# Optimization experiments

Hardware: AMD Instinct MI355X
Metric: run time of the kernel (lower is better)

Reference implementation:

```python
import jax, jax.numpy as jnp
import numpy as np

TAU = 0.2
EPS = 1e-12  # matches torch F.normalize eps


def _l2_normalize(x):
    # F.normalize(x, p=2, dim=1): x / max(||x||, eps)
    norm = jnp.sqrt(jnp.sum(x * x, axis=1, keepdims=True))
    return x / jnp.maximum(norm, EPS)


def setup_inputs() -> dict:
    key = jax.random.key(0)
    k1, k2 = jax.random.split(key)
    N, D = 16384, 256
    z1 = jax.random.normal(k1, (N, D), dtype=jnp.float32)
    z2 = jax.random.normal(k2, (N, D), dtype=jnp.float32)
    return {"z1": z1, "z2": z2}


def reference(z1, z2):
    # semi_loss: f(x) = exp(x / tau) over full cosine-similarity matrix
    h1 = _l2_normalize(z1)
    h2 = _l2_normalize(z2)
    sim = jnp.einsum('nd,md->nm', h1, h2)          # [N, N] cosine similarities
    between = jnp.exp(sim / TAU)                   # f(pair_sim)
    diag = jnp.diagonal(between)                   # positive pairs
    row_sum = jnp.sum(between, axis=1)
    loss = jnp.sum(-jnp.log(diag / (row_sum - diag)))
    return loss
```

## Files before the change

### kernel.cpp

```cpp
#include <hip/hip_runtime.h>
#include <hip/hip_bf16.h>

#define NROWS 16384
#define DDIM  256
#define LOG2E 1.4426950408889634f
#define SCALE 7.213475204444817f

typedef __attribute__((ext_vector_type(4))) float f32x4;
typedef __attribute__((ext_vector_type(2))) float f32x2;
typedef __attribute__((ext_vector_type(4))) int   i32x4;
typedef __attribute__((ext_vector_type(8))) int   i32x8;

#define UNIT_SCALE 0x7F7F7F7F

__global__ __launch_bounds__(256) void prep_kernel(
    const float* __restrict__ z1, const float* __restrict__ z2,
    unsigned char* __restrict__ h1q, unsigned char* __restrict__ h2t,
    float* __restrict__ diag5, float* __restrict__ rowsum) {
  int tid = threadIdx.x;
  int w = tid >> 6, lane = tid & 63;
  int r = blockIdx.x * 4 + w;

  const float4 a = ((const float4*)z1)[r * 64 + lane];
  const float4 b = ((const float4*)z2)[r * 64 + lane];

  float ss1 = a.x * a.x + a.y * a.y + a.z * a.z + a.w * a.w;
  float ss2 = b.x * b.x + b.y * b.y + b.z * b.z + b.w * b.w;
  float dp  = a.x * b.x + a.y * b.y + a.z * b.z + a.w * b.w;
  #pragma unroll
  for (int m = 1; m <= 32; m <<= 1) {
    ss1 += __shfl_xor(ss1, m);
    ss2 += __shfl_xor(ss2, m);
    dp  += __shfl_xor(dp, m);
  }
  float inv1 = 1.0f / fmaxf(sqrtf(ss1), 1e-12f);
  float inv2 = 1.0f / fmaxf(sqrtf(ss2), 1e-12f);
  float s1 = inv1 * SCALE;

  int p1 = __builtin_amdgcn_cvt_pk_fp8_f32(a.x * s1, a.y * s1, 0, false);
  p1     = __builtin_amdgcn_cvt_pk_fp8_f32(a.z * s1, a.w * s1, p1, true);
  int p2 = __builtin_amdgcn_cvt_pk_fp8_f32(b.x * inv2, b.y * inv2, 0, false);
  p2     = __builtin_amdgcn_cvt_pk_fp8_f32(b.z * inv2, b.w * inv2, p2, true);
  ((int*)h1q)[r * 64 + lane] = p1;

  {
    int c = lane >> 2, sub = lane & 3;
    int off = (r >> 4) * 4096 + (c >> 3) * 2048 + (c & 1) * 1024 +
              ((c >> 1) & 3) * 256 + (r & 15) * 16 + sub * 4;
    *(int*)(h2t + off) = p2;
  }

  if (lane == 0) diag5[r] = dp * inv1 * inv2 * 5.0f;
  if (tid < 4) rowsum[blockIdx.x * 4 + tid] = 0.0f;
}

#define CSPL 16

#define LOADSET(B, P0, P1) do { \
  B[0] = *reinterpret_cast<const i32x4*>(P0); \
  B[1] = *reinterpret_cast<const i32x4*>(P0 + 1024); \
  B[2] = *reinterpret_cast<const i32x4*>(P0 + 2048); \
  B[3] = *reinterpret_cast<const i32x4*>(P0 + 3072); \
  B[4] = *reinterpret_cast<const i32x4*>(P1); \
  B[5] = *reinterpret_cast<const i32x4*>(P1 + 1024); \
  B[6] = *reinterpret_cast<const i32x4*>(P1 + 2048); \
  B[7] = *reinterpret_cast<const i32x4*>(P1 + 3072); \
  P0 += 8192; P1 += 8192; } while (0)

#define MFMA_S(Aop, Bop, Cop) \
  __builtin_amdgcn_mfma_scale_f32_16x16x128_f8f6f4( \
      Aop, Bop, Cop, 0, 0, 0, UNIT_SCALE, 0, UNIT_SCALE)

#define COMPUTE(B) do { \
  union { i32x8 v; i32x4 h[2]; } u00, u01, u10, u11; \
  u00.h[0] = B[0]; u00.h[1] = B[1]; u01.h[0] = B[2]; u01.h[1] = B[3]; \
  u10.h[0] = B[4]; u10.h[1] = B[5]; u11.h[0] = B[6]; u11.h[1] = B[7]; \
  f32x4 a0[4], a1[4]; \
  _Pragma("unroll") for (int m = 0; m < 4; ++m) a0[m] = MFMA_S(afr[m][0], u00.v, ZV); \
  _Pragma("unroll") for (int m = 0; m < 4; ++m) a1[m] = MFMA_S(afr[m][0], u10.v, ZV); \
  _Pragma("unroll") for (int m = 0; m < 4; ++m) a0[m] = MFMA_S(afr[m][1], u01.v, a0[m]); \
  _Pragma("unroll") for (int m = 0; m < 4; ++m) a1[m] = MFMA_S(afr[m][1], u11.v, a1[m]); \
  _Pragma("unroll") for (int m = 0; m < 4; ++m) { \
    rs2[m][0] += (f32x2){__builtin_amdgcn_exp2f(a0[m][0]), __builtin_amdgcn_exp2f(a0[m][1])}; \
    rs2[m][1] += (f32x2){__builtin_amdgcn_exp2f(a0[m][2]), __builtin_amdgcn_exp2f(a0[m][3])}; \
    rs2[m][0] += (f32x2){__builtin_amdgcn_exp2f(a1[m][0]), __builtin_amdgcn_exp2f(a1[m][1])}; \
    rs2[m][1] += (f32x2){__builtin_amdgcn_exp2f(a1[m][2]), __builtin_amdgcn_exp2f(a1[m][3])}; \
  } } while (0)

__global__ __launch_bounds__(256) void simexp_kernel(
    const unsigned char* __restrict__ h1q, const unsigned char* __restrict__ h2t,
    float* __restrict__ rowsum) {
  int tid = threadIdx.x, w = tid >> 6, lane = tid & 63;
  int bx = blockIdx.x;
  int rb = bx >> 4;
  int cs = bx & 15;
  int row0 = rb * 256 + w * 64;

  const char* h1b = (const char*)h1q;

  i32x8 afr[4][2];
  #pragma unroll
  for (int m = 0; m < 4; ++m)
    #pragma unroll
    for (int ks = 0; ks < 2; ++ks) {
      int row = row0 + m * 16 + (lane & 15);
      int off = row * 256 + ks * 128 + (lane >> 4) * 32;
      afr[m][ks] = *reinterpret_cast<const i32x8*>(h1b + off);
    }
  #pragma unroll
  for (int m = 0; m < 4; ++m)
    #pragma unroll
    for (int ks = 0; ks < 2; ++ks)
      asm volatile("" : "+v"(afr[m][ks]));

  const char* Bp0 = (const char*)h2t + (size_t)cs * 262144 + lane * 16;
  const char* Bp1 = Bp0 + 4096;

  const f32x4 ZV = {0.f, 0.f, 0.f, 0.f};
  f32x2 rs2[4][2];
  #pragma unroll
  for (int m = 0; m < 4; ++m) {
    rs2[m][0] = (f32x2){0.f, 0.f};
    rs2[m][1] = (f32x2){0.f, 0.f};
  }

  i32x4 bufA[8], bufB[8];
  LOADSET(bufA, Bp0, Bp1);

  for (int jt2 = 0; jt2 < 16; ++jt2) {
    LOADSET(bufB, Bp0, Bp1);
    COMPUTE(bufA);
    LOADSET(bufA, Bp0, Bp1);
    COMPUTE(bufB);
  }

  #pragma unroll
  for (int m = 0; m < 4; ++m)
    #pragma unroll
    for (int p = 0; p < 2; ++p)
      #pragma unroll
      for (int c = 0; c < 2; ++c) {
        float v = rs2[m][p][c];
        v += __shfl_xor(v, 1);
        v += __shfl_xor(v, 2);
        v += __shfl_xor(v, 4);
        v += __shfl_xor(v, 8);
        if ((lane & 15) == 0)
          atomicAdd(&rowsum[row0 + m * 16 + (lane >> 4) * 4 + p * 2 + c], v);
      }
}

__global__ __launch_bounds__(1024) void loss_kernel(
    const float* __restrict__ rowsum, const float* __restrict__ diag5,
    float* __restrict__ out) {
  int tid = threadIdx.x;
  float s = 0.0f;
  for (int i = tid; i < NROWS; i += 1024) {
    float d5 = diag5[i];
    float de = __builtin_amdgcn_exp2f(d5 * LOG2E);
    s += logf(rowsum[i] - de) - d5;
  }
  #pragma unroll
  for (int m = 1; m <= 32; m <<= 1) s += __shfl_xor(s, m);
  __shared__ float wsum[16];
  if ((tid & 63) == 0) wsum[tid >> 6] = s;
  __syncthreads();
  if (tid == 0) {
    float t = 0.0f;
    #pragma unroll
    for (int i = 0; i < 16; ++i) t += wsum[i];
    out[0] = t;
  }
}

extern "C" void kernel_launch(void* const* d_in, const int* in_sizes, int n_in,
                              void* d_out, int out_size, void* d_ws, size_t ws_size,
                              hipStream_t stream) {
  const float* z1 = (const float*)d_in[0];
  const float* z2 = (const float*)d_in[1];

  char* ws = (char*)d_ws;
  unsigned char* h1q = (unsigned char*)(ws);
  unsigned char* h2t = (unsigned char*)(ws + 4194304);
  float* diag5 = (float*)(ws + 8421376);
  float* rowsm = (float*)(ws + 8486912);
  if (ws_size < 8552448) return;

  prep_kernel<<<4096, 256, 0, stream>>>(z1, z2, h1q, h2t, diag5, rowsm);
  simexp_kernel<<<1024, 256, 0, stream>>>(h1q, h2t, rowsm);
  loss_kernel<<<1, 1024, 0, stream>>>(rowsm, diag5, (float*)d_out);
}
```

Before: 93.45 us.

## Software-pipeline MFMA and exp across tiles, cut column splits to four

```diff
diff --git a/kernel.cpp b/kernel.cpp
--- a/kernel.cpp
+++ b/kernel.cpp
@@ -54,7 +54,7 @@
   if (tid < 4) rowsum[blockIdx.x * 4 + tid] = 0.0f;
 }
 
-#define CSPL 16
+#define CSPL 4
 
 #define LOADSET(B, P0, P1) do { \
   B[0] = *reinterpret_cast<const i32x4*>(P0); \
@@ -71,29 +71,42 @@
   __builtin_amdgcn_mfma_scale_f32_16x16x128_f8f6f4( \
       Aop, Bop, Cop, 0, 0, 0, UNIT_SCALE, 0, UNIT_SCALE)
 
-#define COMPUTE(B) do { \
+#define MFMA_TILE(B, ACC) do { \
   union { i32x8 v; i32x4 h[2]; } u00, u01, u10, u11; \
   u00.h[0] = B[0]; u00.h[1] = B[1]; u01.h[0] = B[2]; u01.h[1] = B[3]; \
   u10.h[0] = B[4]; u10.h[1] = B[5]; u11.h[0] = B[6]; u11.h[1] = B[7]; \
-  f32x4 a0[4], a1[4]; \
-  _Pragma("unroll") for (int m = 0; m < 4; ++m) a0[m] = MFMA_S(afr[m][0], u00.v, ZV); \
-  _Pragma("unroll") for (int m = 0; m < 4; ++m) a1[m] = MFMA_S(afr[m][0], u10.v, ZV); \
-  _Pragma("unroll") for (int m = 0; m < 4; ++m) a0[m] = MFMA_S(afr[m][1], u01.v, a0[m]); \
-  _Pragma("unroll") for (int m = 0; m < 4; ++m) a1[m] = MFMA_S(afr[m][1], u11.v, a1[m]); \
-  _Pragma("unroll") for (int m = 0; m < 4; ++m) { \
-    rs2[m][0] += (f32x2){__builtin_amdgcn_exp2f(a0[m][0]), __builtin_amdgcn_exp2f(a0[m][1])}; \
-    rs2[m][1] += (f32x2){__builtin_amdgcn_exp2f(a0[m][2]), __builtin_amdgcn_exp2f(a0[m][3])}; \
-    rs2[m][0] += (f32x2){__builtin_amdgcn_exp2f(a1[m][0]), __builtin_amdgcn_exp2f(a1[m][1])}; \
-    rs2[m][1] += (f32x2){__builtin_amdgcn_exp2f(a1[m][2]), __builtin_amdgcn_exp2f(a1[m][3])}; \
-  } } while (0)
-
-__global__ __launch_bounds__(256) void simexp_kernel(
+  _Pragma("unroll") for (int m = 0; m < 4; ++m) ACC[m]     = MFMA_S(afr[m][0], u00.v, ZV); \
+  _Pragma("unroll") for (int m = 0; m < 4; ++m) ACC[4 + m] = MFMA_S(afr[m][0], u10.v, ZV); \
+  _Pragma("unroll") for (int m = 0; m < 4; ++m) ACC[m]     = MFMA_S(afr[m][1], u01.v, ACC[m]); \
+  _Pragma("unroll") for (int m = 0; m < 4; ++m) ACC[4 + m] = MFMA_S(afr[m][1], u11.v, ACC[4 + m]); \
+} while (0)
+
+#define EXPACC(ACC) do { \
+  _Pragma("unroll") for (int q = 0; q < 8; ++q) { \
+    rs2[q & 3][0] += (f32x2){__builtin_amdgcn_exp2f(ACC[q][0]), \
+                             __builtin_amdgcn_exp2f(ACC[q][1])}; \
+    rs2[q & 3][1] += (f32x2){__builtin_amdgcn_exp2f(ACC[q][2]), \
+                             __builtin_amdgcn_exp2f(ACC[q][3])}; \
+  } \
+} while (0)
+
+#define SGB_TILE() do { \
+  __builtin_amdgcn_sched_group_barrier(0x020, 8, 0); \
+  _Pragma("unroll") for (int i_ = 0; i_ < 16; ++i_) { \
+    __builtin_amdgcn_sched_group_barrier(0x008, 1, 0); \
+    __builtin_amdgcn_sched_group_barrier(0x002, 3, 0); \
+  } \
+} while (0)
+
+__global__ __launch_bounds__(256)
+__attribute__((amdgpu_waves_per_eu(1, 2)))
+void simexp_kernel(
     const unsigned char* __restrict__ h1q, const unsigned char* __restrict__ h2t,
     float* __restrict__ rowsum) {
   int tid = threadIdx.x, w = tid >> 6, lane = tid & 63;
   int bx = blockIdx.x;
-  int rb = bx >> 4;
-  int cs = bx & 15;
+  int rb = bx >> 2;
+  int cs = bx & 3;
   int row0 = rb * 256 + w * 64;
 
   const char* h1b = (const char*)h1q;
@@ -113,7 +126,7 @@
     for (int ks = 0; ks < 2; ++ks)
       asm volatile("" : "+v"(afr[m][ks]));
 
-  const char* Bp0 = (const char*)h2t + (size_t)cs * 262144 + lane * 16;
+  const char* Bp0 = (const char*)h2t + (size_t)cs * 1048576 + lane * 16;
   const char* Bp1 = Bp0 + 4096;
 
   const f32x4 ZV = {0.f, 0.f, 0.f, 0.f};
@@ -125,14 +138,21 @@
   }
 
   i32x4 bufA[8], bufB[8];
+  f32x4 accA[8], accB[8];
+
   LOADSET(bufA, Bp0, Bp1);
 
-  for (int jt2 = 0; jt2 < 16; ++jt2) {
+  for (int k = 0; k < 64; ++k) {
     LOADSET(bufB, Bp0, Bp1);
-    COMPUTE(bufA);
+    MFMA_TILE(bufA, accA);
+    if (k) EXPACC(accB);
+    SGB_TILE();
     LOADSET(bufA, Bp0, Bp1);
-    COMPUTE(bufB);
-  }
+    MFMA_TILE(bufB, accB);
+    EXPACC(accA);
+    SGB_TILE();
+  }
+  EXPACC(accB);
 
   #pragma unroll
   for (int m = 0; m < 4; ++m)
@@ -187,6 +207,6 @@
   if (ws_size < 8552448) return;
 
   prep_kernel<<<4096, 256, 0, stream>>>(z1, z2, h1q, h2t, diag5, rowsm);
-  simexp_kernel<<<1024, 256, 0, stream>>>(h1q, h2t, rowsm);
+  simexp_kernel<<<256, 256, 0, stream>>>(h1q, h2t, rowsm);
   loss_kernel<<<1, 1024, 0, stream>>>(rowsm, diag5, (float*)d_out);
 }
```

Result: slower. 119.2 us (+27.6%).
